# Performance work log

Measured on AMD Instinct MI355X. Metric: run time of the kernel, lower is better.

Reference implementation:

```python
import jax, jax.numpy as jnp
import numpy as np

EPS = 1e-6

def _conv1x1(x, w, bias):
    # x: [b,cin,h,w], w: [cout,cin]
    y = jnp.einsum('bchw,oc->bohw', x, w)
    return y + bias[None, :, None, None]

def _maxpool2(x):
    b, c, h, w = x.shape
    return x.reshape(b, c, h // 2, 2, w // 2, 2).max(axis=(3, 5))

def _up2_align_corners(x):
    # bilinear upsample x2, align_corners=True (matches torch nn.Upsample)
    b, c, h, w = x.shape
    oh, ow = 2 * h, 2 * w
    ys = jnp.linspace(0.0, h - 1.0, oh)
    xs = jnp.linspace(0.0, w - 1.0, ow)
    y0 = jnp.floor(ys).astype(jnp.int32); y1 = jnp.minimum(y0 + 1, h - 1)
    x0 = jnp.floor(xs).astype(jnp.int32); x1 = jnp.minimum(x0 + 1, w - 1)
    ty = (ys - y0).reshape(1, 1, oh, 1)
    tx = (xs - x0).reshape(1, 1, 1, ow)
    r0 = x[:, :, y0, :]; r1 = x[:, :, y1, :]           # [b,c,oh,w]
    v00 = r0[:, :, :, x0]; v01 = r0[:, :, :, x1]       # [b,c,oh,ow]
    v10 = r1[:, :, :, x0]; v11 = r1[:, :, :, x1]
    return (1 - ty) * ((1 - tx) * v00 + tx * v01) + ty * ((1 - tx) * v10 + tx * v11)

def _norm_corr(fm):
    # fm: [b,N,N], indexed [b,p,q]; ReLU then L2-normalize over q for each p
    m = jnp.maximum(fm, 0.0)
    norm = jnp.sqrt(jnp.sum(m * m, axis=2, keepdims=True) + EPS)
    return m / norm

def setup_inputs() -> dict:
    key = jax.random.key(0)
    ks = jax.random.split(key, 8)
    d = {
        'xa': jax.random.normal(ks[0], (8, 256, 64, 64), jnp.float32),
        'xb': jax.random.normal(ks[1], (8, 256, 64, 64), jnp.float32),
        'conv_w': jax.random.normal(ks[2], (1024, 256), jnp.float32) * 0.02,
        'conv_b': jax.random.normal(ks[3], (1024,), jnp.float32) * 0.02,
        'We': jax.random.normal(ks[4], (1024, 1024), jnp.float32) * 0.02,
        'We2': jax.random.normal(ks[5], (1024, 1024), jnp.float32) * 0.02,
        'conv2_w': jax.random.normal(ks[6], (256, 1024), jnp.float32) * 0.02,
        'conv2_b': jax.random.normal(ks[7], (256,), jnp.float32) * 0.02,
    }
    return d

def reference(xa, xb, conv_w, conv_b, We, We2, conv2_w, conv2_b):
    fa = _maxpool2(_conv1x1(xa, conv_w, conv_b))   # [b,c,h,w]
    fb = _maxpool2(_conv1x1(xb, conv_w, conv_b))
    b, c, h, w = fa.shape
    N = h * w
    Fa = fa.reshape(b, c, N)                        # [b,c,N]
    Fb = fb.reshape(b, c, N)
    Fb_t = jnp.swapaxes(Fb, 1, 2)                   # [b,N,c]
    Fa_t = jnp.swapaxes(Fa, 1, 2)
    # fm[b,p,q] = (linear_e(Fb_t) @ Fa)
    fm = jnp.einsum('bpc,cd,bdq->bpq', Fb_t, We.T, Fa)
    Mab = _norm_corr(fm)                            # normalized over q per p
    fm2 = jnp.einsum('bpc,cd,bdq->bpq', Fa_t, We2.T, Fb)
    Mba = _norm_corr(fm2)
    # torch: bmm(corr.view(b,N,N), feat) with corr_flat[b,q,p] = Mn[b,p,q]
    en_a = jnp.einsum('bpq,bpk->bqk', Mab, Fa_t)    # [b,N,c]
    en_b = jnp.einsum('bpq,bpk->bqk', Mba, Fb_t)
    # faithful reinterpretation (torch .view(b,c,h,w) on a [b,N,c] tensor)
    en_a = en_a.reshape(b, c, h, w)
    en_b = en_b.reshape(b, c, h, w)
    en_a = _conv1x1(_up2_align_corners(en_a), conv2_w, conv2_b)
    en_b = _conv1x1(_up2_align_corners(en_b), conv2_w, conv2_b)
    return (en_a, en_b)
```

## Files before the change

kernel.cpp:

```cpp
#include <hip/hip_runtime.h>

typedef unsigned short u16;
typedef short bfrag __attribute__((ext_vector_type(8)));
typedef float facc  __attribute__((ext_vector_type(4)));

__device__ __forceinline__ float bf2f(u16 u) {
    union { unsigned int i; float f; } v; v.i = ((unsigned int)u) << 16; return v.f;
}
__device__ __forceinline__ u16 f2bf(float f) {
    union { float f; unsigned int i; } v; v.f = f;
    unsigned int r = v.i + 0x7FFFu + ((v.i >> 16) & 1u);
    return (u16)(r >> 16);
}

__device__ __forceinline__ void store_out(u16* p, float v)   { *p = f2bf(v); }
__device__ __forceinline__ void store_out(float* p, float v) { *p = v; }

__device__ __forceinline__ void gl2lds16(const u16* g, char* l) {
    __builtin_amdgcn_global_load_lds(
        (const __attribute__((address_space(1))) unsigned int*)g,
        (__attribute__((address_space(3))) unsigned int*)l,
        16, 0, 0);
}

__global__ void cvt4_k(const float* __restrict__ s0, u16* __restrict__ d0,
                       const float* __restrict__ s1, u16* __restrict__ d1,
                       const float* __restrict__ s2, u16* __restrict__ d2,
                       const float* __restrict__ s3, u16* __restrict__ d3) {
    int i = blockIdx.x * blockDim.x + threadIdx.x;
    if (i < 262144)        d0[i] = f2bf(s0[i]);
    else if (i < 1310720)  d1[i - 262144] = f2bf(s1[i - 262144]);
    else if (i < 2359296)  d2[i - 1310720] = f2bf(s2[i - 1310720]);
    else                   d3[i - 2359296] = f2bf(s3[i - 2359296]);
}

__global__ void transpose_in_k(const float* __restrict__ srcA,
                               const float* __restrict__ srcB,
                               u16* __restrict__ dst) {
    __shared__ u16 tile[64][65];
    const long SX = 1048576;
    const int z  = blockIdx.z;
    const int c0 = blockIdx.x * 64;
    const int r0 = blockIdx.y * 64;
    const int x  = threadIdx.x;
    const int y0 = threadIdx.y;
    const float* s = (z < 8 ? srcA : srcB) + (size_t)(z & 7) * SX;
    for (int i = 0; i < 8; ++i) {
        int r = y0 + i * 8;
        tile[r][x] = f2bf(s[(size_t)(r0 + r) * 4096 + c0 + x]);
    }
    __syncthreads();
    u16* d = dst + (size_t)z * SX;
    for (int i = 0; i < 8; ++i) {
        int c = y0 + i * 8;
        d[(size_t)(c0 + c) * 256 + r0 + x] = tile[x][c];
    }
}

template <typename OutT, int MODE, bool PAIRED>
__global__ __launch_bounds__(256)
void gemm_nt(const u16* __restrict__ A0, const u16* __restrict__ A1, long strideA,
             const u16* __restrict__ B0, const u16* __restrict__ B1, long strideBT,
             OutT* __restrict__ C, long strideC, u16* __restrict__ CT,
             const float* __restrict__ bias, int M, int N, int K) {
    constexpr bool POOL = (MODE == 2);
    __shared__ __align__(16) char smem[32768];
    char* As = smem;
    char* Bs = smem + 16384;

    const int gx = gridDim.x, gy = gridDim.y;
    long id = blockIdx.x + (long)gx * (blockIdx.y + (long)gy * blockIdx.z);
    long total = (long)gx * gy * gridDim.z;
    long nid = (id & 7) * (total >> 3) + (id >> 3);
    const int bx = (int)(nid % gx);
    long rr = nid / gx;
    const int by = (int)(rr % gy);
    const int b  = (int)(rr / gy);

    const int m0 = bx * 128;
    const int n0 = by * 128;

    const u16* Ab; const u16* Bb;
    if (PAIRED) {
        const int bl = b & 7;
        Ab = (b < 8 ? A0 : A1) + (size_t)bl * strideA;
        Bb = (b < 8 ? B0 : B1) + (size_t)bl * strideBT;
    } else {
        Ab = A0 + (size_t)b * strideA;
        Bb = B0 + (size_t)b * strideBT;
    }

    const int t    = threadIdx.x;
    const int lane = t & 63;
    const int w    = t >> 6;
    const int wm   = (w & 1) * 64;
    const int wn   = (w >> 1) * 64;
    const int q    = lane >> 4;
    const int ln   = lane & 15;

    const int s0 = w * 64 + lane;
    const int s1 = s0 + 256;
    const int r0s = s0 >> 2, c0s = (s0 & 3) * 8;
    const int r1s = s1 >> 2, c1s = (s1 & 3) * 8;

    const int gr0 = POOL ? ((2 * by + ((r0s >> 1) & 1)) * 64 + (r0s >> 2) * 2 + (r0s & 1))
                         : (n0 + r0s);
    const int gr1 = POOL ? ((2 * by + ((r1s >> 1) & 1)) * 64 + (r1s >> 2) * 2 + (r1s & 1))
                         : (n0 + r1s);

    const u16* pA0 = Ab + (size_t)(m0 + r0s) * K + c0s;
    const u16* pA1 = Ab + (size_t)(m0 + r1s) * K + c1s;
    const u16* pB0 = Bb + (size_t)gr0 * K + c0s;
    const u16* pB1 = Bb + (size_t)gr1 * K + c1s;

    facc acc[4][4];
    for (int i = 0; i < 4; ++i)
        for (int j = 0; j < 4; ++j)
            acc[i][j] = (facc)0.0f;

    const int nK = K >> 6;
    for (int kt = 0; kt < nK; ++kt) {
        const int k0 = kt << 6;
        gl2lds16(pA0 + k0,      As + s0 * 16);
        gl2lds16(pA1 + k0,      As + s1 * 16);
        gl2lds16(pA0 + k0 + 32, As + 8192 + s0 * 16);
        gl2lds16(pA1 + k0 + 32, As + 8192 + s1 * 16);
        gl2lds16(pB0 + k0,      Bs + s0 * 16);
        gl2lds16(pB1 + k0,      Bs + s1 * 16);
        gl2lds16(pB0 + k0 + 32, Bs + 8192 + s0 * 16);
        gl2lds16(pB1 + k0 + 32, Bs + 8192 + s1 * 16);
        __syncthreads();
        for (int j = 0; j < 2; ++j) {
            const char* Aj = As + j * 8192;
            const char* Bj = Bs + j * 8192;
            bfrag af[4], bfr[4];
            for (int mt = 0; mt < 4; ++mt)
                af[mt] = *reinterpret_cast<const bfrag*>(Aj + (wm + mt * 16 + ln) * 64 + q * 16);
            for (int nt = 0; nt < 4; ++nt)
                bfr[nt] = *reinterpret_cast<const bfrag*>(Bj + (wn + nt * 16 + ln) * 64 + q * 16);
            for (int mt = 0; mt < 4; ++mt)
                for (int nt = 0; nt < 4; ++nt)
                    acc[mt][nt] = __builtin_amdgcn_mfma_f32_16x16x32_bf16(af[mt], bfr[nt], acc[mt][nt], 0, 0, 0);
        }
        __syncthreads();
    }

    if (POOL) {
        u16* Cp  = (u16*)C + (size_t)b * strideC;
        u16* CTb = CT + (size_t)b * strideC;
        const int a = ln >> 2;
        for (int mt = 0; mt < 4; ++mt) {
            const int chb = wm + mt * 16 + q * 4;
            float bs0 = bias[m0 + chb + 0];
            float bs1 = bias[m0 + chb + 1];
            float bs2 = bias[m0 + chb + 2];
            float bs3 = bias[m0 + chb + 3];
            for (int nt = 0; nt < 4; ++nt) {
                const int xp = (wn >> 2) + nt * 4 + a;
                float p0 = acc[mt][nt][0] + bs0;
                float p1 = acc[mt][nt][1] + bs1;
                float p2 = acc[mt][nt][2] + bs2;
                float p3 = acc[mt][nt][3] + bs3;
                p0 = fmaxf(p0, __shfl_xor(p0, 1, 64)); p0 = fmaxf(p0, __shfl_xor(p0, 2, 64));
                p1 = fmaxf(p1, __shfl_xor(p1, 1, 64)); p1 = fmaxf(p1, __shfl_xor(p1, 2, 64));
                p2 = fmaxf(p2, __shfl_xor(p2, 1, 64)); p2 = fmaxf(p2, __shfl_xor(p2, 2, 64));
                p3 = fmaxf(p3, __shfl_xor(p3, 1, 64)); p3 = fmaxf(p3, __shfl_xor(p3, 2, 64));
                float s01 = (ln & 1) ? p1 : p0;
                float s23 = (ln & 1) ? p3 : p2;
                float sel = (ln & 2) ? s23 : s01;
                Cp[(size_t)(m0 + chb + (ln & 3)) * 1024 + by * 32 + xp] = f2bf(sel);
                if ((ln & 3) == 0) {
                    uint2 pk;
                    pk.x = (unsigned)f2bf(p0) | ((unsigned)f2bf(p1) << 16);
                    pk.y = (unsigned)f2bf(p2) | ((unsigned)f2bf(p3) << 16);
                    *reinterpret_cast<uint2*>(&CTb[(size_t)(by * 32 + xp) * 1024 + m0 + chb]) = pk;
                }
            }
        }
    } else if (MODE == 0) {
        u16* Cb = (u16*)C + (size_t)b * strideC;
        u16* dump = (u16*)smem;
        for (int mt = 0; mt < 4; ++mt)
            for (int nt = 0; nt < 4; ++nt)
                for (int r = 0; r < 4; ++r)
                    dump[(wm + mt * 16 + q * 4 + r) * 128 + wn + nt * 16 + ln] = f2bf(acc[mt][nt][r]);
        __syncthreads();
        for (int i = 0; i < 8; ++i) {
            const int row = w * 32 + i * 4 + (lane >> 4);
            const uint4 v = *reinterpret_cast<const uint4*>(dump + row * 128 + (lane & 15) * 8);
            *reinterpret_cast<uint4*>(Cb + (size_t)(m0 + row) * N + n0 + (lane & 15) * 8) = v;
        }
    } else {
        OutT* Cb = C + (size_t)b * strideC;
        for (int mt = 0; mt < 4; ++mt) {
            const int rbase = m0 + wm + mt * 16 + q * 4;
            for (int nt = 0; nt < 4; ++nt) {
                const int col = n0 + wn + nt * 16 + ln;
                for (int r = 0; r < 4; ++r)
                    store_out(&Cb[(size_t)(rbase + r) * N + col], acc[mt][nt][r] + bias[rbase + r]);
            }
        }
    }
}

#define BAR8() do { asm volatile("" ::: "memory"); __builtin_amdgcn_s_barrier(); asm volatile("" ::: "memory"); } while (0)
#define VM6() asm volatile("s_waitcnt vmcnt(6)" ::: "memory")
#define VM0() asm volatile("s_waitcnt vmcnt(0)" ::: "memory")

#define LDA8(BUF, MH) \
    _Pragma("unroll") for (int mf = 0; mf < 4; ++mf) { \
        _Pragma("unroll") for (int ks = 0; ks < 2; ++ks) \
            a[mf][ks] = *reinterpret_cast<const bfrag*>(Ab8 + (BUF) * 32768 + \
                (wr * 128 + ((MH) * 4 + mf) * 16 + ln) * 128 + (((ks * 4 + q) ^ ln7) << 4)); }

#define LDB8(BUF, NH) \
    _Pragma("unroll") for (int nf = 0; nf < 2; ++nf) { \
        _Pragma("unroll") for (int ks = 0; ks < 2; ++ks) \
            bb[(NH) * 2 + nf][ks] = *reinterpret_cast<const bfrag*>(Bb8 + (BUF) * 32768 + \
                (wc * 64 + ((NH) * 2 + nf) * 16 + ln) * 128 + (((ks * 4 + q) ^ ln7) << 4)); }

#define MM8(MH, NH) \
    _Pragma("unroll") for (int mf = 0; mf < 4; ++mf) \
    _Pragma("unroll") for (int nf = 0; nf < 2; ++nf) \
    _Pragma("unroll") for (int ks = 0; ks < 2; ++ks) \
        acc[(MH) * 4 + mf][(NH) * 2 + nf] = __builtin_amdgcn_mfma_f32_16x16x32_bf16( \
            a[mf][ks], bb[(NH) * 2 + nf][ks], acc[(MH) * 4 + mf][(NH) * 2 + nf], 0, 0, 0);

#define STA8(KT, BUF, H, R) gl2lds16(pAs + (size_t)((H) * 128 + (R) * 8) * K + (KT) * 64, \
        Ab8 + (BUF) * 32768 + (H) * 16384 + (w * 2 + (R)) * 1024 + lane * 16)
#define STB8(KT, BUF, H, R) gl2lds16(pBs + (size_t)((H) * 128 + (R) * 8) * K + (KT) * 64, \
        Bb8 + (BUF) * 32768 + (H) * 16384 + (w * 2 + (R)) * 1024 + lane * 16)

template <bool PAIRED>
__global__ __launch_bounds__(512, 1)
void gemm8_nt(const u16* __restrict__ A0, const u16* __restrict__ A1, long strideA,
              const u16* __restrict__ B0, const u16* __restrict__ B1, long strideBT,
              u16* __restrict__ C, long strideC, int N, int K) {
    __shared__ __align__(16) char smem8[131072];
    char* Ab8 = smem8;
    char* Bb8 = smem8 + 65536;

    const int gx = gridDim.x, gy = gridDim.y;
    long id = blockIdx.x + (long)gx * (blockIdx.y + (long)gy * blockIdx.z);
    long total = (long)gx * gy * gridDim.z;
    long nid = (id & 7) * (total >> 3) + (id >> 3);
    const int bx = (int)(nid % gx);
    long rr = nid / gx;
    const int by = (int)(rr % gy);
    const int b  = (int)(rr / gy);
    const int m0 = bx * 256, n0 = by * 256;

    const u16* Ab; const u16* Bb;
    if (PAIRED) {
        const int bl = b & 7;
        Ab = (b < 8 ? A0 : A1) + (size_t)bl * strideA;
        Bb = (b < 8 ? B0 : B1) + (size_t)bl * strideBT;
    } else {
        Ab = A0 + (size_t)b * strideA;
        Bb = B0 + (size_t)b * strideBT;
    }

    const int t    = threadIdx.x;
    const int lane = t & 63;
    const int w    = t >> 6;
    const int wr   = w >> 2;
    const int wc   = w & 3;
    const int q    = lane >> 4;
    const int ln   = lane & 15;
    const int ln7  = ln & 7;
    const int l8   = lane >> 3;
    const int l7   = lane & 7;

    const u16* pAs = Ab + (size_t)(m0 + w * 16 + l8) * K + (l7 ^ l8) * 8;
    const u16* pBs = Bb + (size_t)(n0 + w * 16 + l8) * K + (l7 ^ l8) * 8;

    facc acc[8][4];
    #pragma unroll
    for (int i = 0; i < 8; ++i)
        #pragma unroll
        for (int j = 0; j < 4; ++j)
            acc[i][j] = (facc)0.0f;

    bfrag a[4][2];
    bfrag bb[4][2];

    const int nIter = K >> 7;

    STB8(0, 0, 0, 0); STB8(0, 0, 0, 1); STB8(0, 0, 1, 0); STB8(0, 0, 1, 1);
    STA8(0, 0, 0, 0); STA8(0, 0, 0, 1); STA8(0, 0, 1, 0); STA8(0, 0, 1, 1);
    STB8(1, 1, 0, 0); STB8(1, 1, 0, 1); STB8(1, 1, 1, 0); STB8(1, 1, 1, 1);
    STA8(1, 1, 0, 0); STA8(1, 1, 0, 1);
    VM6();
    BAR8();

    for (int i = 0; i < nIter; ++i) {
        const bool more = (i + 1 < nIter);
        const int t1 = 2 * i + 1, t2 = 2 * i + 2, t3 = 2 * i + 3;

        LDA8(0, 0); LDB8(0, 0);
        STA8(t1, 1, 1, 0); STA8(t1, 1, 1, 1);
        BAR8();
        __builtin_amdgcn_s_setprio(1); MM8(0, 0); __builtin_amdgcn_s_setprio(0);
        BAR8();
        LDB8(0, 1);
        BAR8();
        __builtin_amdgcn_s_setprio(1); MM8(0, 1); __builtin_amdgcn_s_setprio(0);
        BAR8();
        LDA8(0, 1);
        if (more) { STB8(t2, 0, 0, 0); STB8(t2, 0, 0, 1); STB8(t2, 0, 1, 0); STB8(t2, 0, 1, 1); }
        BAR8();
        __builtin_amdgcn_s_setprio(1); MM8(1, 0); __builtin_amdgcn_s_setprio(0);
        BAR8();
        if (more) { STA8(t2, 0, 0, 0); STA8(t2, 0, 0, 1); VM6(); } else { VM0(); }
        BAR8();
        __builtin_amdgcn_s_setprio(1); MM8(1, 1); __builtin_amdgcn_s_setprio(0);
        BAR8();
        LDA8(1, 0); LDB8(1, 0);
        if (more) { STA8(t2, 0, 1, 0); STA8(t2, 0, 1, 1); }
        BAR8();
        __builtin_amdgcn_s_setprio(1); MM8(0, 0); __builtin_amdgcn_s_setprio(0);
        BAR8();
        LDB8(1, 1);
        BAR8();
        __builtin_amdgcn_s_setprio(1); MM8(0, 1); __builtin_amdgcn_s_setprio(0);
        BAR8();
        LDA8(1, 1);
        if (more) { STB8(t3, 1, 0, 0); STB8(t3, 1, 0, 1); STB8(t3, 1, 1, 0); STB8(t3, 1, 1, 1); }
        BAR8();
        __builtin_amdgcn_s_setprio(1); MM8(1, 0); __builtin_amdgcn_s_setprio(0);
        BAR8();
        if (more) { STA8(t3, 1, 0, 0); STA8(t3, 1, 0, 1); VM6(); } else { VM0(); }
        BAR8();
        __builtin_amdgcn_s_setprio(1); MM8(1, 1); __builtin_amdgcn_s_setprio(0);
        BAR8();
    }

    u16* dump = (u16*)smem8;
    #pragma unroll
    for (int mf = 0; mf < 8; ++mf)
        #pragma unroll
        for (int nf = 0; nf < 4; ++nf)
            #pragma unroll
            for (int r = 0; r < 4; ++r)
                dump[(wr * 128 + mf * 16 + q * 4 + r) * 256 + wc * 64 + nf * 16 + ln] =
                    f2bf(acc[mf][nf][r]);
    BAR8();
    u16* Cb = C + (size_t)b * strideC;
    #pragma unroll
    for (int it = 0; it < 16; ++it) {
        int linear = t + it * 512;
        int row = linear >> 5, c16 = linear & 31;
        uint4 v = *reinterpret_cast<const uint4*>(dump + row * 256 + c16 * 8);
        *reinterpret_cast<uint4*>(Cb + (size_t)(m0 + row) * N + n0 + c16 * 8) = v;
    }
}

__global__ void norm_rk(const u16* __restrict__ fm, float* __restrict__ rinv) {
    __shared__ float red[4];
    const long row = blockIdx.x;
    const u16* p = fm + row * 1024;
    const int t = threadIdx.x;
    uint2 raw = *reinterpret_cast<const uint2*>(p + t * 4);
    float v0 = fmaxf(bf2f((u16)(raw.x & 0xFFFF)), 0.f);
    float v1 = fmaxf(bf2f((u16)(raw.x >> 16)), 0.f);
    float v2 = fmaxf(bf2f((u16)(raw.y & 0xFFFF)), 0.f);
    float v3 = fmaxf(bf2f((u16)(raw.y >> 16)), 0.f);
    float s = v0 * v0 + v1 * v1 + v2 * v2 + v3 * v3;
    for (int off = 32; off; off >>= 1) s += __shfl_down(s, off, 64);
    if ((t & 63) == 0) red[t >> 6] = s;
    __syncthreads();
    if (t == 0)
        rinv[row] = 1.0f / sqrtf(red[0] + red[1] + red[2] + red[3] + 1e-6f);
}

__global__ void transpose_scale_k(const u16* __restrict__ src,
                                  const float* __restrict__ rinv,
                                  u16* __restrict__ dst) {
    __shared__ u16 tile[64][65];
    const long S = 1048576;
    const int b  = blockIdx.z;
    const int c0 = blockIdx.x * 64;
    const int r0 = blockIdx.y * 64;
    const int x  = threadIdx.x;
    const int y0 = threadIdx.y;
    const u16* s = src + (size_t)b * S;
    const float* rv = rinv + (size_t)b * 1024;
    for (int i = 0; i < 8; ++i) {
        int r = y0 + i * 8;
        float v = fmaxf(bf2f(s[(size_t)(r0 + r) * 1024 + c0 + x]), 0.f) * rv[r0 + r];
        tile[r][x] = f2bf(v);
    }
    __syncthreads();
    u16* d = dst + (size_t)b * S;
    for (int i = 0; i < 8; ++i) {
        int c = y0 + i * 8;
        d[(size_t)(c0 + c) * 1024 + r0 + x] = tile[x][c];
    }
}

__global__ void upsample_k(const float* __restrict__ V, float* __restrict__ out, int total) {
    int idx = blockIdx.x * blockDim.x + threadIdx.x;
    if (idx >= total) return;
    int X  = idx & 63;
    int Y  = (idx >> 6) & 63;
    long bo = idx >> 12;
    const float* p = V + bo * 1024;
    const float sc = 31.0f / 63.0f;
    float ys = Y * sc;
    float xs = X * sc;
    int y0 = (int)ys; int x0 = (int)xs;
    int y1 = y0 + 1; if (y1 > 31) y1 = 31;
    int x1 = x0 + 1; if (x1 > 31) x1 = 31;
    float ty = ys - y0, tx = xs - x0;
    float v00 = p[y0 * 32 + x0], v01 = p[y0 * 32 + x1];
    float v10 = p[y1 * 32 + x0], v11 = p[y1 * 32 + x1];
    out[idx] = (1.f - ty) * ((1.f - tx) * v00 + tx * v01) + ty * ((1.f - tx) * v10 + tx * v11);
}

extern "C" void kernel_launch(void* const* d_in, const int* in_sizes, int n_in,
                              void* d_out, int out_size, void* d_ws, size_t ws_size,
                              hipStream_t stream) {
    const float* xa      = (const float*)d_in[0];
    const float* xb      = (const float*)d_in[1];
    const float* conv_w  = (const float*)d_in[2];
    const float* conv_b  = (const float*)d_in[3];
    const float* We      = (const float*)d_in[4];
    const float* We2     = (const float*)d_in[5];
    const float* conv2_w = (const float*)d_in[6];
    const float* conv2_b = (const float*)d_in[7];
    float* out = (float*)d_out;
    char* ws = (char*)d_ws;

    const long S1M = 1048576;
    const long MiB = 1048576;

    u16*   XT  = (u16*)(ws + 0);
    u16*   T1  = (u16*)(ws + 0);
    u16*   MT  = (u16*)(ws + 0);
    u16*   FA  = (u16*)(ws + 32 * MiB);
    u16*   FB  = (u16*)(ws + 48 * MiB);
    u16*   FAT = (u16*)(ws + 64 * MiB);
    u16*   FBT = (u16*)(ws + 80 * MiB);
    float* V   = (float*)(ws + 64 * MiB);
    u16*   FM  = (u16*)(ws + 96 * MiB);
    u16*   Z   = (u16*)(ws + 96 * MiB);
    u16*   CW  = (u16*)(ws + 128 * MiB);
    u16*   WE  = (u16*)(ws + 128 * MiB + 524288);
    u16*   WE2 = (u16*)(ws + 128 * MiB + 2621440);
    u16*   C2W = (u16*)(ws + 128 * MiB + 4718592);
    float* RIV = (float*)(ws + 128 * MiB + 5242880);

    const dim3 tb64(64, 8);

    cvt4_k<<<10240, 256, 0, stream>>>(conv_w, CW, We, WE, We2, WE2, conv2_w, C2W);

    transpose_in_k<<<dim3(64, 4, 16), tb64, 0, stream>>>(xa, xb, XT);

    gemm_nt<u16, 2, false><<<dim3(8, 32, 16), 256, 0, stream>>>(
        CW, CW, 0, XT, XT, S1M, FA, S1M, FAT, conv_b, 1024, 4096, 256);

    gemm8_nt<true><<<dim3(4, 4, 16), 512, 0, stream>>>(
        FBT, FAT, S1M, WE, WE2, 0, T1, S1M, 1024, 1024);

    gemm8_nt<true><<<dim3(4, 4, 16), 512, 0, stream>>>(
        T1, T1 + 8 * S1M, S1M, FAT, FBT, S1M, FM, S1M, 1024, 1024);

    norm_rk<<<16384, 256, 0, stream>>>(FM, RIV);

    transpose_scale_k<<<dim3(16, 16, 16), tb64, 0, stream>>>(FM, RIV, MT);

    gemm8_nt<true><<<dim3(4, 4, 16), 512, 0, stream>>>(
        FA, FB, S1M, MT, MT + 8 * S1M, S1M, Z, S1M, 1024, 1024);

    gemm_nt<float, 1, false><<<dim3(2, 8, 16), 256, 0, stream>>>(
        C2W, C2W, 0, Z, Z, S1M, V, 256L * 1024, nullptr, conv2_b, 256, 1024, 1024);

    upsample_k<<<65536, 256, 0, stream>>>(V, out, 16 * 256 * 4096);
}
```

Before: 387.2 us.

## Double-buffer conv1x1+maxpool GEMM with swizzled LDS and async prefetch

```diff
diff --git a/kernel.cpp b/kernel.cpp
--- a/kernel.cpp
+++ b/kernel.cpp
@@ -63,7 +63,6 @@
              const u16* __restrict__ B0, const u16* __restrict__ B1, long strideBT,
              OutT* __restrict__ C, long strideC, u16* __restrict__ CT,
              const float* __restrict__ bias, int M, int N, int K) {
-    constexpr bool POOL = (MODE == 2);
     __shared__ __align__(16) char smem[32768];
     char* As = smem;
     char* Bs = smem + 16384;
@@ -103,15 +102,10 @@
     const int r0s = s0 >> 2, c0s = (s0 & 3) * 8;
     const int r1s = s1 >> 2, c1s = (s1 & 3) * 8;
 
-    const int gr0 = POOL ? ((2 * by + ((r0s >> 1) & 1)) * 64 + (r0s >> 2) * 2 + (r0s & 1))
-                         : (n0 + r0s);
-    const int gr1 = POOL ? ((2 * by + ((r1s >> 1) & 1)) * 64 + (r1s >> 2) * 2 + (r1s & 1))
-                         : (n0 + r1s);
-
     const u16* pA0 = Ab + (size_t)(m0 + r0s) * K + c0s;
     const u16* pA1 = Ab + (size_t)(m0 + r1s) * K + c1s;
-    const u16* pB0 = Bb + (size_t)gr0 * K + c0s;
-    const u16* pB1 = Bb + (size_t)gr1 * K + c1s;
+    const u16* pB0 = Bb + (size_t)(n0 + r0s) * K + c0s;
+    const u16* pB1 = Bb + (size_t)(n0 + r1s) * K + c1s;
 
     facc acc[4][4];
     for (int i = 0; i < 4; ++i)
@@ -145,39 +139,7 @@
         __syncthreads();
     }
 
-    if (POOL) {
-        u16* Cp  = (u16*)C + (size_t)b * strideC;
-        u16* CTb = CT + (size_t)b * strideC;
-        const int a = ln >> 2;
-        for (int mt = 0; mt < 4; ++mt) {
-            const int chb = wm + mt * 16 + q * 4;
-            float bs0 = bias[m0 + chb + 0];
-            float bs1 = bias[m0 + chb + 1];
-            float bs2 = bias[m0 + chb + 2];
-            float bs3 = bias[m0 + chb + 3];
-            for (int nt = 0; nt < 4; ++nt) {
-                const int xp = (wn >> 2) + nt * 4 + a;
-                float p0 = acc[mt][nt][0] + bs0;
-                float p1 = acc[mt][nt][1] + bs1;
-                float p2 = acc[mt][nt][2] + bs2;
-                float p3 = acc[mt][nt][3] + bs3;
-                p0 = fmaxf(p0, __shfl_xor(p0, 1, 64)); p0 = fmaxf(p0, __shfl_xor(p0, 2, 64));
-                p1 = fmaxf(p1, __shfl_xor(p1, 1, 64)); p1 = fmaxf(p1, __shfl_xor(p1, 2, 64));
-                p2 = fmaxf(p2, __shfl_xor(p2, 1, 64)); p2 = fmaxf(p2, __shfl_xor(p2, 2, 64));
-                p3 = fmaxf(p3, __shfl_xor(p3, 1, 64)); p3 = fmaxf(p3, __shfl_xor(p3, 2, 64));
-                float s01 = (ln & 1) ? p1 : p0;
-                float s23 = (ln & 1) ? p3 : p2;
-                float sel = (ln & 2) ? s23 : s01;
-                Cp[(size_t)(m0 + chb + (ln & 3)) * 1024 + by * 32 + xp] = f2bf(sel);
-                if ((ln & 3) == 0) {
-                    uint2 pk;
-                    pk.x = (unsigned)f2bf(p0) | ((unsigned)f2bf(p1) << 16);
-                    pk.y = (unsigned)f2bf(p2) | ((unsigned)f2bf(p3) << 16);
-                    *reinterpret_cast<uint2*>(&CTb[(size_t)(by * 32 + xp) * 1024 + m0 + chb]) = pk;
-                }
-            }
-        }
-    } else if (MODE == 0) {
+    if (MODE == 0) {
         u16* Cb = (u16*)C + (size_t)b * strideC;
         u16* dump = (u16*)smem;
         for (int mt = 0; mt < 4; ++mt)
@@ -203,6 +165,126 @@
     }
 }
 
+#define BARP() do { asm volatile("" ::: "memory"); __builtin_amdgcn_s_barrier(); asm volatile("" ::: "memory"); } while (0)
+#define VM4P() asm volatile("s_waitcnt vmcnt(4)" ::: "memory")
+#define VM0P() asm volatile("s_waitcnt vmcnt(0)" ::: "memory")
+
+#define STGP(KT, BUF) do { \
+    gl2lds16(pA0 + (KT) * 32, smem + (BUF) * 16384 + s0 * 16); \
+    gl2lds16(pA1 + (KT) * 32, smem + (BUF) * 16384 + s1 * 16); \
+    gl2lds16(pB0 + (KT) * 32, smem + (BUF) * 16384 + 8192 + s0 * 16); \
+    gl2lds16(pB1 + (KT) * 32, smem + (BUF) * 16384 + 8192 + s1 * 16); \
+} while (0)
+
+__global__ __launch_bounds__(256)
+void gemm2p_pool(const u16* __restrict__ A, const u16* __restrict__ B0, long strideBT,
+                 u16* __restrict__ C, long strideC, u16* __restrict__ CT,
+                 const float* __restrict__ bias, int K) {
+    __shared__ __align__(16) char smem[32768];
+
+    const int gx = gridDim.x, gy = gridDim.y;
+    long id = blockIdx.x + (long)gx * (blockIdx.y + (long)gy * blockIdx.z);
+    long total = (long)gx * gy * gridDim.z;
+    long nid = (id & 7) * (total >> 3) + (id >> 3);
+    const int bx = (int)(nid % gx);
+    long rr = nid / gx;
+    const int by = (int)(rr % gy);
+    const int b  = (int)(rr / gy);
+    const int m0 = bx * 128;
+
+    const u16* Bb = B0 + (size_t)b * strideBT;
+
+    const int t    = threadIdx.x;
+    const int lane = t & 63;
+    const int w    = t >> 6;
+    const int wm   = (w & 1) * 64;
+    const int wn   = (w >> 1) * 64;
+    const int q    = lane >> 4;
+    const int ln   = lane & 15;
+
+    const int s0 = w * 64 + lane;
+    const int s1 = s0 + 256;
+    const int r0s = s0 >> 2, c0s = s0 & 3;
+    const int r1s = s1 >> 2, c1s = s1 & 3;
+    const int x0 = (r0s >> 1) & 3, x1 = (r1s >> 1) & 3;
+    const int gr0 = (2 * by + ((r0s >> 1) & 1)) * 64 + (r0s >> 2) * 2 + (r0s & 1);
+    const int gr1 = (2 * by + ((r1s >> 1) & 1)) * 64 + (r1s >> 2) * 2 + (r1s & 1);
+
+    const u16* pA0 = A  + (size_t)(m0 + r0s) * K + (c0s ^ x0) * 8;
+    const u16* pA1 = A  + (size_t)(m0 + r1s) * K + (c1s ^ x1) * 8;
+    const u16* pB0 = Bb + (size_t)gr0 * K + (c0s ^ x0) * 8;
+    const u16* pB1 = Bb + (size_t)gr1 * K + (c1s ^ x1) * 8;
+
+    facc acc[4][4];
+    #pragma unroll
+    for (int i = 0; i < 4; ++i)
+        #pragma unroll
+        for (int j = 0; j < 4; ++j)
+            acc[i][j] = (facc)0.0f;
+
+    const int nK = K >> 5;
+
+    STGP(0, 0);
+    for (int kt = 0; kt < nK; ++kt) {
+        const bool more = (kt + 1 < nK);
+        if (more) { STGP(kt + 1, (kt + 1) & 1); VM4P(); } else { VM0P(); }
+        BARP();
+        const char* Aj = smem + (kt & 1) * 16384;
+        const char* Bj = Aj + 8192;
+        bfrag af[4], bfr[4];
+        #pragma unroll
+        for (int mt = 0; mt < 4; ++mt) {
+            const int row = wm + mt * 16 + ln;
+            af[mt] = *reinterpret_cast<const bfrag*>(Aj + row * 64 + ((q ^ ((row >> 1) & 3)) << 4));
+        }
+        #pragma unroll
+        for (int nt = 0; nt < 4; ++nt) {
+            const int row = wn + nt * 16 + ln;
+            bfr[nt] = *reinterpret_cast<const bfrag*>(Bj + row * 64 + ((q ^ ((row >> 1) & 3)) << 4));
+        }
+        #pragma unroll
+        for (int mt = 0; mt < 4; ++mt)
+            #pragma unroll
+            for (int nt = 0; nt < 4; ++nt)
+                acc[mt][nt] = __builtin_amdgcn_mfma_f32_16x16x32_bf16(af[mt], bfr[nt], acc[mt][nt], 0, 0, 0);
+        BARP();
+    }
+
+    u16* Cp  = C  + (size_t)b * strideC;
+    u16* CTb = CT + (size_t)b * strideC;
+    const int a = ln >> 2;
+    #pragma unroll
+    for (int mt = 0; mt < 4; ++mt) {
+        const int chb = wm + mt * 16 + q * 4;
+        float bs0 = bias[m0 + chb + 0];
+        float bs1 = bias[m0 + chb + 1];
+        float bs2 = bias[m0 + chb + 2];
+        float bs3 = bias[m0 + chb + 3];
+        #pragma unroll
+        for (int nt = 0; nt < 4; ++nt) {
+            const int xp = (wn >> 2) + nt * 4 + a;
+            float p0 = acc[mt][nt][0] + bs0;
+            float p1 = acc[mt][nt][1] + bs1;
+            float p2 = acc[mt][nt][2] + bs2;
+            float p3 = acc[mt][nt][3] + bs3;
+            p0 = fmaxf(p0, __shfl_xor(p0, 1, 64)); p0 = fmaxf(p0, __shfl_xor(p0, 2, 64));
+            p1 = fmaxf(p1, __shfl_xor(p1, 1, 64)); p1 = fmaxf(p1, __shfl_xor(p1, 2, 64));
+            p2 = fmaxf(p2, __shfl_xor(p2, 1, 64)); p2 = fmaxf(p2, __shfl_xor(p2, 2, 64));
+            p3 = fmaxf(p3, __shfl_xor(p3, 1, 64)); p3 = fmaxf(p3, __shfl_xor(p3, 2, 64));
+            float s01 = (ln & 1) ? p1 : p0;
+            float s23 = (ln & 1) ? p3 : p2;
+            float sel = (ln & 2) ? s23 : s01;
+            Cp[(size_t)(m0 + chb + (ln & 3)) * 1024 + by * 32 + xp] = f2bf(sel);
+            if ((ln & 3) == 0) {
+                uint2 pk;
+                pk.x = (unsigned)f2bf(p0) | ((unsigned)f2bf(p1) << 16);
+                pk.y = (unsigned)f2bf(p2) | ((unsigned)f2bf(p3) << 16);
+                *reinterpret_cast<uint2*>(&CTb[(size_t)(by * 32 + xp) * 1024 + m0 + chb]) = pk;
+            }
+        }
+    }
+}
+
 #define BAR8() do { asm volatile("" ::: "memory"); __builtin_amdgcn_s_barrier(); asm volatile("" ::: "memory"); } while (0)
 #define VM6() asm volatile("s_waitcnt vmcnt(6)" ::: "memory")
 #define VM0() asm volatile("s_waitcnt vmcnt(0)" ::: "memory")
@@ -456,8 +538,8 @@
 
     transpose_in_k<<<dim3(64, 4, 16), tb64, 0, stream>>>(xa, xb, XT);
 
-    gemm_nt<u16, 2, false><<<dim3(8, 32, 16), 256, 0, stream>>>(
-        CW, CW, 0, XT, XT, S1M, FA, S1M, FAT, conv_b, 1024, 4096, 256);
+    gemm2p_pool<<<dim3(8, 32, 16), 256, 0, stream>>>(
+        CW, XT, S1M, FA, S1M, FAT, conv_b, 256);
 
     gemm8_nt<true><<<dim3(4, 4, 16), 512, 0, stream>>>(
         FBT, FAT, S1M, WE, WE2, 0, T1, S1M, 1024, 1024);
```

New measurement: 369.8 us. 4.5% less time.
